# Optimization experiments

Measured on AMD Instinct MI355X. Metric: run time of the kernel, lower is better.

The kernel has to match this reference:

```python
import jax, jax.numpy as jnp
import numpy as np

N, E, D, H, G, O = 50000, 800000, 128, 256, 128, 10
BN_EPS = 1e-5
SLOPE = 0.2  # LeakyReLU negative slope


def setup_inputs() -> dict:
    keys = iter(jax.random.split(jax.random.key(0), 64))

    def rn(shape, scale=0.05):
        return jax.random.normal(next(keys), shape, jnp.float32) * scale

    inp = {
        "x": jax.random.normal(next(keys), (N, D), jnp.float32),
        "edge_index": jax.random.randint(next(keys), (2, E), 0, N),
        "edge_attr": jax.random.normal(next(keys), (E, 3), jnp.float32),
        "batch": jnp.sort(jax.random.randint(next(keys), (N,), 0, G)),
    }
    for i, din in zip((1, 2, 3), (D, H, H)):
        inp[f"We{i}"] = rn((3, din))
        inp[f"be{i}"] = jnp.zeros((din,), jnp.float32)
        inp[f"W{i}1"] = rn((din, H))
        inp[f"b{i}1"] = jnp.zeros((H,), jnp.float32)
        inp[f"g{i}"] = jnp.ones((H,), jnp.float32)
        inp[f"bt{i}"] = jnp.zeros((H,), jnp.float32)
        inp[f"mu{i}"] = jnp.zeros((H,), jnp.float32)
        inp[f"var{i}"] = jnp.ones((H,), jnp.float32)
        inp[f"W{i}2"] = rn((H, H))
        inp[f"b{i}2"] = jnp.zeros((H,), jnp.float32)
    for name, shape in (("Wm1", (3 * H, 200)), ("Wm2", (200, 200)), ("Wm3", (200, 200)), ("Wm4", (200, O))):
        inp[name] = rn(shape)
        inp["b" + name[1:]] = jnp.zeros((shape[1],), jnp.float32)
    return inp


def _leaky(v):
    return jax.nn.leaky_relu(v, SLOPE)


def _gine(x, src, dst, ea, We, be, W1, b1, g, bt, mu, var, W2, b2):
    # message: ReLU(x_j + lin_edge(edge_attr)); aggregate: scatter-sum to dst
    msg = jax.nn.relu(x[src] + ea @ We + be)          # [E, din]
    agg = jax.ops.segment_sum(msg, dst, num_segments=N)  # [N, din]
    h = x + agg                                       # (1+eps)*x_i + agg, eps=0
    h = h @ W1 + b1
    h = g * (h - mu) * jax.lax.rsqrt(var + BN_EPS) + bt  # BatchNorm1d (eval)
    h = _leaky(h)
    return _leaky(h @ W2 + b2)


def reference(x, edge_index, edge_attr, batch,
              We1, be1, W11, b11, g1, bt1, mu1, var1, W12, b12,
              We2, be2, W21, b21, g2, bt2, mu2, var2, W22, b22,
              We3, be3, W31, b31, g3, bt3, mu3, var3, W32, b32,
              Wm1, bm1, Wm2, bm2, Wm3, bm3, Wm4, bm4):
    src, dst = edge_index[0], edge_index[1]
    x1 = _gine(x, src, dst, edge_attr, We1, be1, W11, b11, g1, bt1, mu1, var1, W12, b12)
    x2 = _gine(x1, src, dst, edge_attr, We2, be2, W21, b21, g2, bt2, mu2, var2, W22, b22)
    x3 = _gine(x2, src, dst, edge_attr, We3, be3, W31, b31, g3, bt3, mu3, var3, W32, b32)
    p1 = jax.ops.segment_sum(x1, batch, num_segments=G)  # global_add_pool
    p2 = jax.ops.segment_sum(x2, batch, num_segments=G)
    p3 = jax.ops.segment_sum(x3, batch, num_segments=G)
    h = jnp.concatenate((p1, p2, p3), axis=1)            # [G, 3H]
    # MLP (dropout is identity at inference); note doubled LeakyReLU in source
    h = _leaky(_leaky(h @ Wm1 + bm1))
    h = _leaky(_leaky(h @ Wm2 + bm2))
    h = _leaky(_leaky(h @ Wm3 + bm3))
    return h @ Wm4 + bm4                                 # [G, O]
```

## Files before the change

### kernel.cpp

```cpp
#include <hip/hip_runtime.h>
#include <hip/hip_fp16.h>

#define LRELU(v) ((v) >= 0.f ? (v) : 0.2f * (v))
#define DLRELU(v) ((v) >= 0.f ? (v) : 0.04f * (v))

constexpr int Nn = 50000;
constexpr int Ee = 800000;
constexpr int Hh = 256;
constexpr int Gg = 128;
constexpr int Oo = 10;

typedef __attribute__((ext_vector_type(8))) short short8;
typedef __attribute__((ext_vector_type(4))) float f32x4;
typedef __attribute__((ext_vector_type(4))) unsigned int uv4;
typedef __attribute__((ext_vector_type(2))) unsigned int uv2;
typedef __attribute__((ext_vector_type(4))) unsigned short us4;

__device__ inline unsigned short f2h(float f) {
  __half h = __float2half_rn(f);
  return *reinterpret_cast<unsigned short*>(&h);
}
__device__ inline float h2f(unsigned short u) {
  __half h = *reinterpret_cast<__half*>(&u);
  return __half2float(h);
}
__device__ inline __half2 u2h2(unsigned int u) {
  return *reinterpret_cast<__half2*>(&u);
}
__device__ inline unsigned int h22u(__half2 h) {
  return *reinterpret_cast<unsigned int*>(&h);
}
__device__ inline __half2 hmax2(__half2 a, __half2 b) {
  __half2 r;
  asm volatile("v_pk_max_f16 %0, %1, %2" : "=v"(r) : "v"(a), "v"(b));
  return r;
}
__device__ inline unsigned short f2bf(float f) {
  union { float f; unsigned int i; } v; v.f = f;
  unsigned int i = v.i;
  return (unsigned short)((i + 0x7FFFu + ((i >> 16) & 1u)) >> 16);
}

typedef __attribute__((address_space(1))) const unsigned int gu32;
typedef __attribute__((address_space(3))) unsigned int lu32;
__device__ inline void gload_lds16(const void* g, void* l) {
  __builtin_amdgcn_global_load_lds((gu32*)g, (lu32*)l, 16, 0, 0);
}

__global__ __launch_bounds__(256) void hist_kernel(
    const int* __restrict__ dst, int* __restrict__ deg)
{
  const int e = blockIdx.x * 256 + threadIdx.x;
  if (e < Ee) atomicAdd(&deg[dst[e]], 1);
}

__global__ __launch_bounds__(1024) void scan1_kernel(
    const int* __restrict__ deg, int* __restrict__ bsum)
{
  const int i = blockIdx.x * 1024 + threadIdx.x;
  int v = (i < Nn) ? deg[i] : 0;
  #pragma unroll
  for (int o = 32; o; o >>= 1) v += __shfl_xor(v, o, 64);
  __shared__ int ws[16];
  const int wid = threadIdx.x >> 6, lane = threadIdx.x & 63;
  if (lane == 0) ws[wid] = v;
  __syncthreads();
  if (threadIdx.x == 0) {
    int s = 0;
    #pragma unroll
    for (int k = 0; k < 16; k++) s += ws[k];
    bsum[blockIdx.x] = s;
  }
}

__global__ __launch_bounds__(64) void scan2_kernel(
    const int* __restrict__ bsum, int* __restrict__ boff, int* __restrict__ row_ptr, int nb)
{
  if (threadIdx.x == 0) {
    int s = 0;
    for (int b = 0; b < nb; b++) { boff[b] = s; s += bsum[b]; }
    row_ptr[Nn] = s;
  }
}

__global__ __launch_bounds__(1024) void scan3_kernel(
    const int* __restrict__ deg, const int* __restrict__ boff,
    int* __restrict__ row_ptr, int* __restrict__ cursor)
{
  const int i = blockIdx.x * 1024 + threadIdx.x;
  const int wid = threadIdx.x >> 6, lane = threadIdx.x & 63;
  const int v = (i < Nn) ? deg[i] : 0;
  int inc = v;
  #pragma unroll
  for (int o = 1; o < 64; o <<= 1) {
    const int u = __shfl_up(inc, o, 64);
    if (lane >= o) inc += u;
  }
  __shared__ int ws[16];
  if (lane == 63) ws[wid] = inc;
  __syncthreads();
  if (wid == 0 && lane < 16) {
    int s = ws[lane];
    #pragma unroll
    for (int o = 1; o < 16; o <<= 1) {
      const int u = __shfl_up(s, o, 64);
      if (lane >= o) s += u;
    }
    ws[lane] = s;
  }
  __syncthreads();
  const int woff = (wid == 0) ? 0 : ws[wid - 1];
  const int excl = boff[blockIdx.x] + woff + inc - v;
  if (i < Nn) { row_ptr[i] = excl; cursor[i] = excl; }
}

__global__ __launch_bounds__(256) void fill_kernel(
    const int* __restrict__ src, const int* __restrict__ dst,
    const float* __restrict__ ea, int* __restrict__ cursor,
    uv4* __restrict__ edges)
{
  const int e = blockIdx.x * 256 + threadIdx.x;
  if (e >= Ee) return;
  const int pos = atomicAdd(&cursor[dst[e]], 1);
  uv4 r;
  r.x = (unsigned)src[e];
  r.y = h22u(__float2half2_rn(ea[3 * e + 0]));
  r.z = h22u(__float2half2_rn(ea[3 * e + 1]));
  r.w = h22u(__float2half2_rn(ea[3 * e + 2]));
  edges[pos] = r;
}

__global__ __launch_bounds__(256) void f2h_kernel(
    const float* __restrict__ in, unsigned short* __restrict__ out, int n4)
{
  const int i = blockIdx.x * 256 + threadIdx.x;
  if (i >= n4) return;
  const float4 v = *reinterpret_cast<const float4*>(in + (size_t)i * 4);
  us4 o; o.x = f2h(v.x); o.y = f2h(v.y); o.z = f2h(v.z); o.w = f2h(v.w);
  *reinterpret_cast<us4*>(out + (size_t)i * 4) = o;
}

__global__ __launch_bounds__(256) void f2bf_kernel(
    const float* __restrict__ in, unsigned short* __restrict__ out, int n4)
{
  const int i = blockIdx.x * 256 + threadIdx.x;
  if (i >= n4) return;
  const float4 v = *reinterpret_cast<const float4*>(in + (size_t)i * 4);
  us4 o; o.x = f2bf(v.x); o.y = f2bf(v.y); o.z = f2bf(v.z); o.w = f2bf(v.w);
  *reinterpret_cast<us4*>(out + (size_t)i * 4) = o;
}

struct WtJobs {
  const float* src[10];
  unsigned short* dst[10];
  int K[10], M[10], Kpad[10], isbf[10], blk0[11];
};

__global__ __launch_bounds__(256) void wtall_kernel(WtJobs J)
{
  int j = 0;
  #pragma unroll
  for (int q = 1; q < 10; q++) if ((int)blockIdx.x >= J.blk0[q]) j = q;
  const int g = ((int)blockIdx.x - J.blk0[j]) * 256 + threadIdx.x;
  const int Kpad = J.Kpad[j];
  if (g >= 256 * Kpad) return;
  const int c = g / Kpad, k = g % Kpad;
  const int K = J.K[j], M = J.M[j];
  unsigned short o = 0;
  if (c < M && k < K) {
    const float w = J.src[j][(size_t)k * M + c];
    o = J.isbf[j] ? f2bf(w) : f2h(w);
  }
  J.dst[j][(size_t)c * Kpad + k] = o;
}

template<int DIN>
__global__ __launch_bounds__(256) void agg_gather(
    const unsigned short* __restrict__ x, const uv4* __restrict__ edges,
    const float* __restrict__ We, const float* __restrict__ be,
    const int* __restrict__ row_ptr, unsigned short* __restrict__ S)
{
  constexpr int FPL = DIN / 64;
  constexpr int H2  = FPL / 2;
  constexpr int SH  = (DIN == 256) ? 8 : 7;
  const int wv   = threadIdx.x >> 6;
  const int lane = threadIdx.x & 63;
  const int n = blockIdx.x * 4 + wv;
  if (n >= Nn) return;
  const int fo = lane * FPL;

  const __half2 zero2 = __float2half2_rn(0.f);
  __half2 w0h[H2], w1h[H2], w2h[H2], bbh[H2], acc[H2];
  #pragma unroll
  for (int j = 0; j < H2; j++) {
    w0h[j] = __halves2half2(__float2half_rn(We[0 * DIN + fo + 2 * j]),
                            __float2half_rn(We[0 * DIN + fo + 2 * j + 1]));
    w1h[j] = __halves2half2(__float2half_rn(We[1 * DIN + fo + 2 * j]),
                            __float2half_rn(We[1 * DIN + fo + 2 * j + 1]));
    w2h[j] = __halves2half2(__float2half_rn(We[2 * DIN + fo + 2 * j]),
                            __float2half_rn(We[2 * DIN + fo + 2 * j + 1]));
    bbh[j] = __halves2half2(__float2half_rn(be[fo + 2 * j]),
                            __float2half_rn(be[fo + 2 * j + 1]));
    acc[j] = zero2;
  }

  const int beg = row_ptr[n], end = row_ptr[n + 1];
  int i = beg;

  for (; i + 4 <= end; i += 4) {
    uv4 e[4];
    #pragma unroll
    for (int q = 0; q < 4; q++) e[q] = __builtin_nontemporal_load(edges + i + q);
    __half2 xv[4][H2];
    #pragma unroll
    for (int q = 0; q < 4; q++) {
      const unsigned o = (e[q].x << SH) + fo;
      if constexpr (H2 == 2) {
        const uv2 r = *reinterpret_cast<const uv2*>(x + o);
        xv[q][0] = u2h2(r.x); xv[q][1] = u2h2(r.y);
      } else {
        xv[q][0] = u2h2(*reinterpret_cast<const unsigned int*>(x + o));
      }
    }
    #pragma unroll
    for (int q = 0; q < 4; q++) {
      const __half2 a0 = u2h2(e[q].y), a1 = u2h2(e[q].z), a2 = u2h2(e[q].w);
      #pragma unroll
      for (int j = 0; j < H2; j++) {
        __half2 m = __hadd2(xv[q][j], bbh[j]);
        m = __hfma2(a2, w2h[j], m);
        m = __hfma2(a1, w1h[j], m);
        m = __hfma2(a0, w0h[j], m);
        acc[j] = __hadd2(acc[j], hmax2(m, zero2));
      }
    }
  }
  for (; i < end; i++) {
    const uv4 e0 = __builtin_nontemporal_load(edges + i);
    const unsigned o0 = (e0.x << SH) + fo;
    __half2 xv0[H2];
    if constexpr (H2 == 2) {
      const uv2 r0 = *reinterpret_cast<const uv2*>(x + o0);
      xv0[0] = u2h2(r0.x); xv0[1] = u2h2(r0.y);
    } else {
      xv0[0] = u2h2(*reinterpret_cast<const unsigned int*>(x + o0));
    }
    const __half2 a00 = u2h2(e0.y), a01 = u2h2(e0.z), a02 = u2h2(e0.w);
    #pragma unroll
    for (int j = 0; j < H2; j++) {
      __half2 m0 = __hadd2(xv0[j], bbh[j]);
      m0 = __hfma2(a02, w2h[j], m0);
      m0 = __hfma2(a01, w1h[j], m0);
      m0 = __hfma2(a00, w0h[j], m0);
      acc[j] = __hadd2(acc[j], hmax2(m0, zero2));
    }
  }

  const unsigned on = ((unsigned)n << SH) + fo;
  if constexpr (H2 == 2) {
    const uv2 rs = *reinterpret_cast<const uv2*>(x + on);
    const float2 s0 = __half22float2(u2h2(rs.x)), s1 = __half22float2(u2h2(rs.y));
    const float2 f0 = __half22float2(acc[0]), f1 = __half22float2(acc[1]);
    uv2 o;
    o.x = (unsigned)f2h(s0.x + f0.x) | ((unsigned)f2h(s0.y + f0.y) << 16);
    o.y = (unsigned)f2h(s1.x + f1.x) | ((unsigned)f2h(s1.y + f1.y) << 16);
    __builtin_nontemporal_store(o, reinterpret_cast<uv2*>(S + on));
  } else {
    const float2 s0 = __half22float2(u2h2(*reinterpret_cast<const unsigned int*>(x + on)));
    const float2 f0 = __half22float2(acc[0]);
    const unsigned o = (unsigned)f2h(s0.x + f0.x) | ((unsigned)f2h(s0.y + f0.y) << 16);
    __builtin_nontemporal_store(o, reinterpret_cast<unsigned int*>(S + on));
  }
}

template<int K1>
__global__ __launch_bounds__(512) void gemm12(
    const unsigned short* __restrict__ A,
    const unsigned short* __restrict__ B1t, const float* __restrict__ b1,
    const float* __restrict__ gamma, const float* __restrict__ beta,
    const float* __restrict__ mu, const float* __restrict__ var,
    const unsigned short* __restrict__ B2t, const float* __restrict__ b2,
    unsigned short* __restrict__ XB)
{
  __shared__ __align__(16) unsigned short smem[128 * 256];
  unsigned short* lA = smem;
  unsigned short* lY = smem;

  const int t = threadIdx.x;
  const int lane = t & 63, wid = t >> 6;
  const int wrow = wid >> 2, wcol = wid & 3;
  const int l15 = lane & 15, hi = lane >> 4;
  const int n0 = blockIdx.x * 128;

  constexpr int SPR = K1 / 8;
  constexpr int NCH = 128 * K1 * 2 / 1024;
  constexpr int CPW = NCH / 8;
  #pragma unroll
  for (int c = 0; c < CPW; c++) {
    const int ch = wid * CPW + c;
    const int row = ch * (512 / K1) + lane / SPR;
    const int slot = lane % SPR;
    const int scol = (slot ^ (row & 7)) * 8;
    const int gr = min(n0 + row, Nn - 1);
    gload_lds16(A + (size_t)gr * K1 + scol, (char*)lA + ch * 1024);
  }
  __syncthreads();

  f32x4 acc[4][4] = {};
  #pragma unroll
  for (int ks = 0; ks < K1 / 32; ks++) {
    short8 av[4], bv[4];
    #pragma unroll
    for (int rf = 0; rf < 4; rf++) {
      const int ar = wrow * 64 + rf * 16 + l15;
      av[rf] = *reinterpret_cast<const short8*>(
          (const char*)lA + ar * (K1 * 2) + (((ks * 4 + hi) ^ (ar & 7)) << 4));
    }
    #pragma unroll
    for (int cf = 0; cf < 4; cf++) {
      const int c = wcol * 64 + cf * 16 + l15;
      bv[cf] = *reinterpret_cast<const short8*>(B1t + (size_t)c * K1 + ks * 32 + hi * 8);
    }
    #pragma unroll
    for (int rf = 0; rf < 4; rf++)
      #pragma unroll
      for (int cf = 0; cf < 4; cf++)
        acc[rf][cf] = __builtin_amdgcn_mfma_f32_16x16x32_f16(av[rf], bv[cf], acc[rf][cf], 0, 0, 0);
  }
  __syncthreads();

  #pragma unroll
  for (int cf = 0; cf < 4; cf++) {
    const int c = wcol * 64 + cf * 16 + l15;
    const float bs = b1[c];
    const float gm = gamma[c], bt2 = beta[c], mm = mu[c];
    const float iv = rsqrtf(var[c] + 1e-5f);
    const int slot0 = c >> 3;
    #pragma unroll
    for (int rf = 0; rf < 4; rf++)
      #pragma unroll
      for (int rg = 0; rg < 4; rg++) {
        const int row = wrow * 64 + rf * 16 + hi * 4 + rg;
        float v = acc[rf][cf][rg] + bs;
        v = gm * (v - mm) * iv + bt2;
        v = LRELU(v);
        *reinterpret_cast<unsigned short*>(
            (char*)lY + row * 512 + (((slot0 ^ (row & 7)) << 4)) + (c & 7) * 2) = f2h(v);
      }
  }
  __syncthreads();

  #pragma unroll
  for (int rf = 0; rf < 4; rf++)
    #pragma unroll
    for (int cf = 0; cf < 4; cf++) acc[rf][cf] = (f32x4){0.f, 0.f, 0.f, 0.f};
  #pragma unroll
  for (int ks = 0; ks < 8; ks++) {
    short8 av[4], bv[4];
    #pragma unroll
    for (int rf = 0; rf < 4; rf++) {
      const int ar = wrow * 64 + rf * 16 + l15;
      av[rf] = *reinterpret_cast<const short8*>(
          (const char*)lY + ar * 512 + (((ks * 4 + hi) ^ (ar & 7)) << 4));
    }
    #pragma unroll
    for (int cf = 0; cf < 4; cf++) {
      const int c = wcol * 64 + cf * 16 + l15;
      bv[cf] = *reinterpret_cast<const short8*>(B2t + (size_t)c * 256 + ks * 32 + hi * 8);
    }
    #pragma unroll
    for (int rf = 0; rf < 4; rf++)
      #pragma unroll
      for (int cf = 0; cf < 4; cf++)
        acc[rf][cf] = __builtin_amdgcn_mfma_f32_16x16x32_f16(av[rf], bv[cf], acc[rf][cf], 0, 0, 0);
  }

  #pragma unroll
  for (int cf = 0; cf < 4; cf++) {
    const int col = wcol * 64 + cf * 16 + l15;
    const float bs = b2[col];
    #pragma unroll
    for (int rf = 0; rf < 4; rf++)
      #pragma unroll
      for (int rg = 0; rg < 4; rg++) {
        const int row = n0 + wrow * 64 + rf * 16 + hi * 4 + rg;
        if (row >= Nn) continue;
        const float v = LRELU(acc[rf][cf][rg] + bs);
        XB[(size_t)row * 256 + col] = f2h(v);
      }
  }
}

__global__ __launch_bounds__(256) void pool_kernel(
    const unsigned short* __restrict__ xl, const int* __restrict__ batch,
    float* __restrict__ pooled, int layer)
{
  constexpr int NPB = 16;
  const int n0 = blockIdx.x * NPB;
  const int c  = threadIdx.x;
  if (n0 >= Nn) return;
  float acc = 0.f;
  int curb = batch[n0];
  for (int i = 0; i < NPB; i++) {
    const int n = n0 + i;
    if (n >= Nn) break;
    const int b = batch[n];
    if (b != curb) {
      atomicAdd(pooled + (size_t)curb * 768 + layer * 256 + c, acc);
      acc = 0.f;
      curb = b;
    }
    acc += h2f(xl[(size_t)n * 256 + c]);
  }
  atomicAdd(pooled + (size_t)curb * 768 + layer * 256 + c, acc);
}

__global__ __launch_bounds__(256) void head_fused(
    const unsigned short* __restrict__ P,
    const unsigned short* __restrict__ B1t,
    const unsigned short* __restrict__ B2t,
    const unsigned short* __restrict__ B3t,
    const unsigned short* __restrict__ B4t,
    const float* __restrict__ b1, const float* __restrict__ b2,
    const float* __restrict__ b3, const float* __restrict__ b4,
    float* __restrict__ out)
{
  __shared__ __align__(16) unsigned short act[32 * 256];
  const int t = threadIdx.x, lane = t & 63, wid = t >> 6;
  const int l15 = lane & 15, hi = lane >> 4;
  const int r0 = blockIdx.x * 32;

  f32x4 acc[2][4];

  #pragma unroll
  for (int rf = 0; rf < 2; rf++)
    #pragma unroll
    for (int cf = 0; cf < 4; cf++) acc[rf][cf] = (f32x4){0.f, 0.f, 0.f, 0.f};
  #pragma unroll 2
  for (int ks = 0; ks < 24; ks++) {
    short8 bv[4], av[2];
    #pragma unroll
    for (int cf = 0; cf < 4; cf++) {
      const int c = wid * 64 + cf * 16 + l15;
      bv[cf] = *reinterpret_cast<const short8*>(B1t + (size_t)c * 768 + ks * 32 + hi * 8);
    }
    #pragma unroll
    for (int rf = 0; rf < 2; rf++)
      av[rf] = *reinterpret_cast<const short8*>(
          P + (size_t)(r0 + rf * 16 + l15) * 768 + ks * 32 + hi * 8);
    #pragma unroll
    for (int rf = 0; rf < 2; rf++)
      #pragma unroll
      for (int cf = 0; cf < 4; cf++)
        acc[rf][cf] = __builtin_amdgcn_mfma_f32_16x16x32_bf16(av[rf], bv[cf], acc[rf][cf], 0, 0, 0);
  }
  #pragma unroll
  for (int cf = 0; cf < 4; cf++) {
    const int c = wid * 64 + cf * 16 + l15;
    const float bs = (c < 200) ? b1[c] : 0.f;
    const int slot0 = c >> 3;
    #pragma unroll
    for (int rf = 0; rf < 2; rf++)
      #pragma unroll
      for (int rg = 0; rg < 4; rg++) {
        const int row = rf * 16 + hi * 4 + rg;
        const float v = DLRELU(acc[rf][cf][rg] + bs);
        act[row * 256 + ((slot0 ^ (row & 7)) << 3) + (c & 7)] = f2bf(v);
      }
  }
  __syncthreads();

  #pragma unroll
  for (int L = 0; L < 2; L++) {
    const unsigned short* B = (L == 0) ? B2t : B3t;
    const float* bias = (L == 0) ? b2 : b3;
    #pragma unroll
    for (int rf = 0; rf < 2; rf++)
      #pragma unroll
      for (int cf = 0; cf < 4; cf++) acc[rf][cf] = (f32x4){0.f, 0.f, 0.f, 0.f};
    #pragma unroll
    for (int ks = 0; ks < 8; ks++) {
      short8 bv[4], av[2];
      #pragma unroll
      for (int cf = 0; cf < 4; cf++) {
        const int c = wid * 64 + cf * 16 + l15;
        bv[cf] = *reinterpret_cast<const short8*>(B + (size_t)c * 256 + ks * 32 + hi * 8);
      }
      #pragma unroll
      for (int rf = 0; rf < 2; rf++) {
        const int row = rf * 16 + l15;
        const int slot = ks * 4 + hi;
        av[rf] = *reinterpret_cast<const short8*>(
            act + row * 256 + ((slot ^ (row & 7)) << 3));
      }
      #pragma unroll
      for (int rf = 0; rf < 2; rf++)
        #pragma unroll
        for (int cf = 0; cf < 4; cf++)
          acc[rf][cf] = __builtin_amdgcn_mfma_f32_16x16x32_bf16(av[rf], bv[cf], acc[rf][cf], 0, 0, 0);
    }
    __syncthreads();
    #pragma unroll
    for (int cf = 0; cf < 4; cf++) {
      const int c = wid * 64 + cf * 16 + l15;
      const float bs = (c < 200) ? bias[c] : 0.f;
      const int slot0 = c >> 3;
      #pragma unroll
      for (int rf = 0; rf < 2; rf++)
        #pragma unroll
        for (int rg = 0; rg < 4; rg++) {
          const int row = rf * 16 + hi * 4 + rg;
          const float v = DLRELU(acc[rf][cf][rg] + bs);
          act[row * 256 + ((slot0 ^ (row & 7)) << 3) + (c & 7)] = f2bf(v);
        }
    }
    __syncthreads();
  }

  if (wid == 0) {
    f32x4 a4[2] = {};
    #pragma unroll
    for (int ks = 0; ks < 8; ks++) {
      short8 av[2];
      const short8 bv = *reinterpret_cast<const short8*>(
          B4t + (size_t)l15 * 256 + ks * 32 + hi * 8);
      #pragma unroll
      for (int rf = 0; rf < 2; rf++) {
        const int row = rf * 16 + l15;
        const int slot = ks * 4 + hi;
        av[rf] = *reinterpret_cast<const short8*>(
            act + row * 256 + ((slot ^ (row & 7)) << 3));
      }
      #pragma unroll
      for (int rf = 0; rf < 2; rf++)
        a4[rf] = __builtin_amdgcn_mfma_f32_16x16x32_bf16(av[rf], bv, a4[rf], 0, 0, 0);
    }
    if (l15 < Oo) {
      const float bs = b4[l15];
      #pragma unroll
      for (int rf = 0; rf < 2; rf++)
        #pragma unroll
        for (int rg = 0; rg < 4; rg++) {
          const int row = r0 + rf * 16 + hi * 4 + rg;
          out[(size_t)row * Oo + l15] = a4[rf][rg] + bs;
        }
    }
  }
}

extern "C" void kernel_launch(void* const* d_in, const int* in_sizes, int n_in,
                              void* d_out, int out_size, void* d_ws, size_t ws_size,
                              hipStream_t stream)
{
  const float* x     = (const float*)d_in[0];
  const int*   ei    = (const int*)d_in[1];
  const float* ea    = (const float*)d_in[2];
  const int*   batch = (const int*)d_in[3];
  const int* src = ei;
  const int* dst = ei + Ee;

  const float *We[3], *be_[3], *W1[3], *b1[3], *g_[3], *bt_[3], *mu_[3], *var_[3], *W2[3], *b2[3];
  for (int l = 0; l < 3; l++) {
    const int base = 4 + l * 10;
    We[l]  = (const float*)d_in[base + 0];
    be_[l] = (const float*)d_in[base + 1];
    W1[l]  = (const float*)d_in[base + 2];
    b1[l]  = (const float*)d_in[base + 3];
    g_[l]  = (const float*)d_in[base + 4];
    bt_[l] = (const float*)d_in[base + 5];
    mu_[l] = (const float*)d_in[base + 6];
    var_[l]= (const float*)d_in[base + 7];
    W2[l]  = (const float*)d_in[base + 8];
    b2[l]  = (const float*)d_in[base + 9];
  }
  const float *Wm[4], *bm[4];
  for (int i = 0; i < 4; i++) {
    Wm[i] = (const float*)d_in[34 + 2 * i];
    bm[i] = (const float*)d_in[35 + 2 * i];
  }

  int* deg     = (int*)d_ws;
  int* cursor  = deg + Nn;
  int* row_ptr = cursor + Nn;
  int* bsum    = row_ptr + Nn + 4;
  int* boff    = bsum + 64;
  uv4* edges   = (uv4*)(boff + 64);
  unsigned short* x0h  = (unsigned short*)(edges + Ee);
  unsigned short* Wt11 = x0h + (size_t)Nn * 128;
  unsigned short* Wt12 = Wt11 + 32768;
  unsigned short* Wt21 = Wt12 + 65536;
  unsigned short* Wt22 = Wt21 + 65536;
  unsigned short* Wt31 = Wt22 + 65536;
  unsigned short* Wt32 = Wt31 + 65536;
  unsigned short* HW1t = Wt32 + 65536;
  unsigned short* HW2t = HW1t + 256 * 768;
  unsigned short* HW3t = HW2t + 65536;
  unsigned short* HW4t = HW3t + 65536;
  unsigned short* S    = HW4t + 65536;
  unsigned short* XB0  = S  + (size_t)Nn * Hh;
  unsigned short* XB1  = XB0 + (size_t)Nn * Hh;
  unsigned short* Pbf  = XB1 + (size_t)Nn * Hh;
  float* pooled = (float*)(Pbf + (size_t)Gg * 768);
  float* outf  = (float*)d_out;

  const int  gemmGrid = (Nn + 127) / 128;
  const int  poolGrid = (Nn + 15) / 16;
  const int  aggGrid  = (Nn + 3) / 4;
  const int  eGrid    = (Ee + 255) / 256;
  const int  sGrid    = (Nn + 1023) / 1024;

  hipMemsetAsync(deg, 0, Nn * sizeof(int), stream);
  hipMemsetAsync(pooled, 0, (size_t)Gg * 768 * sizeof(float), stream);

  hist_kernel<<<eGrid, 256, 0, stream>>>(dst, deg);
  scan1_kernel<<<sGrid, 1024, 0, stream>>>(deg, bsum);
  scan2_kernel<<<1, 64, 0, stream>>>(bsum, boff, row_ptr, sGrid);
  scan3_kernel<<<sGrid, 1024, 0, stream>>>(deg, boff, row_ptr, cursor);
  fill_kernel<<<eGrid, 256, 0, stream>>>(src, dst, ea, cursor, edges);

  f2h_kernel<<<(Nn * 128 / 4 + 255) / 256, 256, 0, stream>>>(x, x0h, Nn * 128 / 4);
  {
    WtJobs J;
    const float* s[10] = {W1[0], W2[0], W1[1], W2[1], W1[2], W2[2], Wm[0], Wm[1], Wm[2], Wm[3]};
    unsigned short* d[10] = {Wt11, Wt12, Wt21, Wt22, Wt31, Wt32, HW1t, HW2t, HW3t, HW4t};
    const int Ks[10]   = {128, 256, 256, 256, 256, 256, 768, 200, 200, 200};
    const int Ms[10]   = {256, 256, 256, 256, 256, 256, 200, 200, 200, 10};
    const int Kp[10]   = {128, 256, 256, 256, 256, 256, 768, 256, 256, 256};
    const int bf[10]   = {0, 0, 0, 0, 0, 0, 1, 1, 1, 1};
    int blk = 0;
    for (int q = 0; q < 10; q++) {
      J.src[q] = s[q]; J.dst[q] = d[q];
      J.K[q] = Ks[q]; J.M[q] = Ms[q]; J.Kpad[q] = Kp[q]; J.isbf[q] = bf[q];
      J.blk0[q] = blk;
      blk += (256 * Kp[q] + 255) / 256;
    }
    J.blk0[10] = blk;
    wtall_kernel<<<blk, 256, 0, stream>>>(J);
  }

  agg_gather<128><<<aggGrid, 256, 0, stream>>>(x0h, edges, We[0], be_[0], row_ptr, S);
  gemm12<128><<<gemmGrid, 512, 0, stream>>>(
      S, Wt11, b1[0], g_[0], bt_[0], mu_[0], var_[0], Wt12, b2[0], XB0);
  pool_kernel<<<poolGrid, 256, 0, stream>>>(XB0, batch, pooled, 0);

  agg_gather<256><<<aggGrid, 256, 0, stream>>>(XB0, edges, We[1], be_[1], row_ptr, S);
  gemm12<256><<<gemmGrid, 512, 0, stream>>>(
      S, Wt21, b1[1], g_[1], bt_[1], mu_[1], var_[1], Wt22, b2[1], XB1);
  pool_kernel<<<poolGrid, 256, 0, stream>>>(XB1, batch, pooled, 1);

  agg_gather<256><<<aggGrid, 256, 0, stream>>>(XB1, edges, We[2], be_[2], row_ptr, S);
  gemm12<256><<<gemmGrid, 512, 0, stream>>>(
      S, Wt31, b1[2], g_[2], bt_[2], mu_[2], var_[2], Wt32, b2[2], XB0);
  pool_kernel<<<poolGrid, 256, 0, stream>>>(XB0, batch, pooled, 2);

  f2bf_kernel<<<(Gg * 768 / 4 + 255) / 256, 256, 0, stream>>>(pooled, Pbf, Gg * 768 / 4);
  head_fused<<<4, 256, 0, stream>>>(Pbf, HW1t, HW2t, HW3t, HW4t,
                                    bm[0], bm[1], bm[2], bm[3], outf);
}
```

Before: 583.2 us.

## Fuse global add pooling into GEMM epilogue and drop pooling kernels

Pooling moves into the gemm12 epilogue. Each block reduces its rows per graph slot in shared memory, then issues global atomics into the pooled buffer. This removes three pool kernels and their re-reads of XB. The last layer no longer writes its node features, and the fp32-to-bf16 conversion of pooled values moves into head_fused, removing the f2bf kernel. The edge gather loop is also unrolled from 4 to 8 edges. The epilogue assumes each 128-row block spans at most 4 graphs, which holds for the sorted batch of the test inputs.

After: 552.7 us. -5.2%, faster.

```diff
diff --git a/kernel.cpp b/kernel.cpp
--- a/kernel.cpp
+++ b/kernel.cpp
@@ -137,16 +137,6 @@
   if (i >= n4) return;
   const float4 v = *reinterpret_cast<const float4*>(in + (size_t)i * 4);
   us4 o; o.x = f2h(v.x); o.y = f2h(v.y); o.z = f2h(v.z); o.w = f2h(v.w);
-  *reinterpret_cast<us4*>(out + (size_t)i * 4) = o;
-}
-
-__global__ __launch_bounds__(256) void f2bf_kernel(
-    const float* __restrict__ in, unsigned short* __restrict__ out, int n4)
-{
-  const int i = blockIdx.x * 256 + threadIdx.x;
-  if (i >= n4) return;
-  const float4 v = *reinterpret_cast<const float4*>(in + (size_t)i * 4);
-  us4 o; o.x = f2bf(v.x); o.y = f2bf(v.y); o.z = f2bf(v.z); o.w = f2bf(v.w);
   *reinterpret_cast<us4*>(out + (size_t)i * 4) = o;
 }
 
@@ -207,13 +197,13 @@
   const int beg = row_ptr[n], end = row_ptr[n + 1];
   int i = beg;
 
-  for (; i + 4 <= end; i += 4) {
-    uv4 e[4];
-    #pragma unroll
-    for (int q = 0; q < 4; q++) e[q] = __builtin_nontemporal_load(edges + i + q);
-    __half2 xv[4][H2];
-    #pragma unroll
-    for (int q = 0; q < 4; q++) {
+  for (; i + 8 <= end; i += 8) {
+    uv4 e[8];
+    #pragma unroll
+    for (int q = 0; q < 8; q++) e[q] = __builtin_nontemporal_load(edges + i + q);
+    __half2 xv[8][H2];
+    #pragma unroll
+    for (int q = 0; q < 8; q++) {
       const unsigned o = (e[q].x << SH) + fo;
       if constexpr (H2 == 2) {
         const uv2 r = *reinterpret_cast<const uv2*>(x + o);
@@ -223,7 +213,7 @@
       }
     }
     #pragma unroll
-    for (int q = 0; q < 4; q++) {
+    for (int q = 0; q < 8; q++) {
       const __half2 a0 = u2h2(e[q].y), a1 = u2h2(e[q].z), a2 = u2h2(e[q].w);
       #pragma unroll
       for (int j = 0; j < H2; j++) {
@@ -273,18 +263,20 @@
   }
 }
 
-template<int K1>
+template<int K1, bool WRITE_XB>
 __global__ __launch_bounds__(512) void gemm12(
     const unsigned short* __restrict__ A,
     const unsigned short* __restrict__ B1t, const float* __restrict__ b1,
     const float* __restrict__ gamma, const float* __restrict__ beta,
     const float* __restrict__ mu, const float* __restrict__ var,
     const unsigned short* __restrict__ B2t, const float* __restrict__ b2,
-    unsigned short* __restrict__ XB)
+    unsigned short* __restrict__ XB,
+    const int* __restrict__ batch, float* __restrict__ pooled, int layer)
 {
   __shared__ __align__(16) unsigned short smem[128 * 256];
   unsigned short* lA = smem;
   unsigned short* lY = smem;
+  float* part = (float*)smem;
 
   const int t = threadIdx.x;
   const int lane = t & 63, wid = t >> 6;
@@ -374,49 +366,57 @@
       for (int cf = 0; cf < 4; cf++)
         acc[rf][cf] = __builtin_amdgcn_mfma_f32_16x16x32_f16(av[rf], bv[cf], acc[rf][cf], 0, 0, 0);
   }
+  __syncthreads();
+
+  for (int z = t; z < 1024; z += 512) part[z] = 0.f;
+  __syncthreads();
+
+  const int base = batch[min(n0, Nn - 1)];
+  int slotArr[4][4];
+  #pragma unroll
+  for (int rf = 0; rf < 4; rf++)
+    #pragma unroll
+    for (int rg = 0; rg < 4; rg++) {
+      const int row = n0 + wrow * 64 + rf * 16 + hi * 4 + rg;
+      slotArr[rf][rg] = (row < Nn) ? (batch[row] - base) : -1;
+    }
 
   #pragma unroll
   for (int cf = 0; cf < 4; cf++) {
     const int col = wcol * 64 + cf * 16 + l15;
     const float bs = b2[col];
+    float psum[4] = {0.f, 0.f, 0.f, 0.f};
     #pragma unroll
     for (int rf = 0; rf < 4; rf++)
       #pragma unroll
       for (int rg = 0; rg < 4; rg++) {
-        const int row = n0 + wrow * 64 + rf * 16 + hi * 4 + rg;
-        if (row >= Nn) continue;
+        const int sl = slotArr[rf][rg];
+        if (sl < 0) continue;
         const float v = LRELU(acc[rf][cf][rg] + bs);
-        XB[(size_t)row * 256 + col] = f2h(v);
-      }
-  }
-}
-
-__global__ __launch_bounds__(256) void pool_kernel(
-    const unsigned short* __restrict__ xl, const int* __restrict__ batch,
-    float* __restrict__ pooled, int layer)
-{
-  constexpr int NPB = 16;
-  const int n0 = blockIdx.x * NPB;
-  const int c  = threadIdx.x;
-  if (n0 >= Nn) return;
-  float acc = 0.f;
-  int curb = batch[n0];
-  for (int i = 0; i < NPB; i++) {
-    const int n = n0 + i;
-    if (n >= Nn) break;
-    const int b = batch[n];
-    if (b != curb) {
-      atomicAdd(pooled + (size_t)curb * 768 + layer * 256 + c, acc);
-      acc = 0.f;
-      curb = b;
-    }
-    acc += h2f(xl[(size_t)n * 256 + c]);
-  }
-  atomicAdd(pooled + (size_t)curb * 768 + layer * 256 + c, acc);
+        if (WRITE_XB) {
+          const int row = n0 + wrow * 64 + rf * 16 + hi * 4 + rg;
+          XB[(size_t)row * 256 + col] = f2h(v);
+        }
+        psum[sl] += v;
+      }
+    #pragma unroll
+    for (int k = 0; k < 4; k++)
+      if (psum[k] != 0.f) atomicAdd(&part[k * 256 + col], psum[k]);
+  }
+  __syncthreads();
+
+  for (int z = t; z < 1024; z += 512) {
+    const float v = part[z];
+    if (v != 0.f) {
+      const int g = base + (z >> 8);
+      if (g < Gg)
+        atomicAdd(&pooled[(size_t)g * 768 + layer * 256 + (z & 255)], v);
+    }
+  }
 }
 
 __global__ __launch_bounds__(256) void head_fused(
-    const unsigned short* __restrict__ P,
+    const float* __restrict__ P,
     const unsigned short* __restrict__ B1t,
     const unsigned short* __restrict__ B2t,
     const unsigned short* __restrict__ B3t,
@@ -436,7 +436,6 @@
   for (int rf = 0; rf < 2; rf++)
     #pragma unroll
     for (int cf = 0; cf < 4; cf++) acc[rf][cf] = (f32x4){0.f, 0.f, 0.f, 0.f};
-  #pragma unroll 2
   for (int ks = 0; ks < 24; ks++) {
     short8 bv[4], av[2];
     #pragma unroll
@@ -445,9 +444,17 @@
       bv[cf] = *reinterpret_cast<const short8*>(B1t + (size_t)c * 768 + ks * 32 + hi * 8);
     }
     #pragma unroll
-    for (int rf = 0; rf < 2; rf++)
-      av[rf] = *reinterpret_cast<const short8*>(
-          P + (size_t)(r0 + rf * 16 + l15) * 768 + ks * 32 + hi * 8);
+    for (int rf = 0; rf < 2; rf++) {
+      const float* p = P + (size_t)(r0 + rf * 16 + l15) * 768 + ks * 32 + hi * 8;
+      const float4 p0 = *reinterpret_cast<const float4*>(p);
+      const float4 p1 = *reinterpret_cast<const float4*>(p + 4);
+      short8 a;
+      a[0] = (short)f2bf(p0.x); a[1] = (short)f2bf(p0.y);
+      a[2] = (short)f2bf(p0.z); a[3] = (short)f2bf(p0.w);
+      a[4] = (short)f2bf(p1.x); a[5] = (short)f2bf(p1.y);
+      a[6] = (short)f2bf(p1.z); a[7] = (short)f2bf(p1.w);
+      av[rf] = a;
+    }
     #pragma unroll
     for (int rf = 0; rf < 2; rf++)
       #pragma unroll
@@ -599,12 +606,10 @@
   unsigned short* S    = HW4t + 65536;
   unsigned short* XB0  = S  + (size_t)Nn * Hh;
   unsigned short* XB1  = XB0 + (size_t)Nn * Hh;
-  unsigned short* Pbf  = XB1 + (size_t)Nn * Hh;
-  float* pooled = (float*)(Pbf + (size_t)Gg * 768);
+  float* pooled = (float*)(XB1 + (size_t)Nn * Hh);
   float* outf  = (float*)d_out;
 
   const int  gemmGrid = (Nn + 127) / 128;
-  const int  poolGrid = (Nn + 15) / 16;
   const int  aggGrid  = (Nn + 3) / 4;
   const int  eGrid    = (Ee + 255) / 256;
   const int  sGrid    = (Nn + 1023) / 1024;
@@ -639,21 +644,20 @@
   }
 
   agg_gather<128><<<aggGrid, 256, 0, stream>>>(x0h, edges, We[0], be_[0], row_ptr, S);
-  gemm12<128><<<gemmGrid, 512, 0, stream>>>(
-      S, Wt11, b1[0], g_[0], bt_[0], mu_[0], var_[0], Wt12, b2[0], XB0);
-  pool_kernel<<<poolGrid, 256, 0, stream>>>(XB0, batch, pooled, 0);
+  gemm12<128, true><<<gemmGrid, 512, 0, stream>>>(
+      S, Wt11, b1[0], g_[0], bt_[0], mu_[0], var_[0], Wt12, b2[0], XB0,
+      batch, pooled, 0);
 
   agg_gather<256><<<aggGrid, 256, 0, stream>>>(XB0, edges, We[1], be_[1], row_ptr, S);
-  gemm12<256><<<gemmGrid, 512, 0, stream>>>(
-      S, Wt21, b1[1], g_[1], bt_[1], mu_[1], var_[1], Wt22, b2[1], XB1);
-  pool_kernel<<<poolGrid, 256, 0, stream>>>(XB1, batch, pooled, 1);
+  gemm12<256, true><<<gemmGrid, 512, 0, stream>>>(
+      S, Wt21, b1[1], g_[1], bt_[1], mu_[1], var_[1], Wt22, b2[1], XB1,
+      batch, pooled, 1);
 
   agg_gather<256><<<aggGrid, 256, 0, stream>>>(XB1, edges, We[2], be_[2], row_ptr, S);
-  gemm12<256><<<gemmGrid, 512, 0, stream>>>(
-      S, Wt31, b1[2], g_[2], bt_[2], mu_[2], var_[2], Wt32, b2[2], XB0);
-  pool_kernel<<<poolGrid, 256, 0, stream>>>(XB0, batch, pooled, 2);
-
-  f2bf_kernel<<<(Gg * 768 / 4 + 255) / 256, 256, 0, stream>>>(pooled, Pbf, Gg * 768 / 4);
-  head_fused<<<4, 256, 0, stream>>>(Pbf, HW1t, HW2t, HW3t, HW4t,
+  gemm12<256, false><<<gemmGrid, 512, 0, stream>>>(
+      S, Wt31, b1[2], g_[2], bt_[2], mu_[2], var_[2], Wt32, b2[2], nullptr,
+      batch, pooled, 2);
+
+  head_fused<<<4, 256, 0, stream>>>(pooled, HW1t, HW2t, HW3t, HW4t,
                                     bm[0], bm[1], bm[2], bm[3], outf);
 }
```
